# Performance work log

Measured on AMD Instinct MI355X. Metric: run time of the kernel, lower is better.

## Reference

```python
import jax, jax.numpy as jnp
import numpy as np
import math

D_MODEL = 1024
N_HEADS = 16
D_HEAD = D_MODEL // N_HEADS
B, T = 2, 2048


def setup_inputs() -> dict:
    key = jax.random.key(0)
    ks = jax.random.split(key, 5)
    x = jax.random.normal(ks[0], (B, T, D_MODEL), dtype=jnp.float32)
    W_qkv = jax.random.normal(ks[1], (D_MODEL, 3 * D_MODEL), dtype=jnp.float32) * 0.02
    b_qkv = jnp.zeros((3 * D_MODEL,), dtype=jnp.float32)
    W_g = jax.random.normal(ks[2], (N_HEADS, D_HEAD, D_HEAD), dtype=jnp.float32) * 0.02
    W_out = jax.random.normal(ks[3], (D_MODEL, D_MODEL), dtype=jnp.float32) * 0.02
    b_out = jnp.zeros((D_MODEL,), dtype=jnp.float32)
    return {"x": x, "W_qkv": W_qkv, "b_qkv": b_qkv, "W_g": W_g, "W_out": W_out, "b_out": b_out}


def reference(x, W_qkv, b_qkv, W_g, W_out, b_out):
    b, t, d = x.shape
    h, dh = N_HEADS, D_HEAD
    qkv = x @ W_qkv + b_qkv                         # (B,T,3D)
    q, k, v = jnp.split(qkv, 3, axis=-1)
    # (B,T,D) -> (B,H,T,dh)
    q = q.reshape(b, t, h, dh).transpose(0, 2, 1, 3)
    k = k.reshape(b, t, h, dh).transpose(0, 2, 1, 3)
    v = v.reshape(b, t, h, dh).transpose(0, 2, 1, 3)
    scale = 1.0 / math.sqrt(dh)
    scores = jnp.einsum('bhtd,bhsd->bhts', q, k) * scale   # (B,H,T,T)
    causal = jnp.tril(jnp.ones((t, t), dtype=bool))
    scores = jnp.where(causal, scores, jnp.float32(-jnp.inf))
    attn = jax.nn.softmax(scores, axis=-1)
    # query-conditioned bilinear value gate (applied at each position)
    g = jax.nn.sigmoid(jnp.einsum('bhtd,hde->bhte', q, W_g))  # (B,H,T,dh)
    v = g * v
    out = jnp.einsum('bhts,bhsd->bhtd', attn, v)             # (B,H,T,dh)
    out = out.transpose(0, 2, 1, 3).reshape(b, t, d)
    return out @ W_out + b_out
```

## Files before the change

kernel.cpp:

```cpp
#include <hip/hip_runtime.h>
#include <hip/hip_bf16.h>

typedef unsigned short ushortT;
typedef __bf16 bf16x8 __attribute__((ext_vector_type(8)));
typedef __bf16 bf16x4 __attribute__((ext_vector_type(4)));
typedef float f32x4 __attribute__((ext_vector_type(4)));

#define T_SEQ 2048
#define DH 64
#define NH 16
#define DM 1024
#define TD 3072
#define BATCH 2
#define LOG2E 1.44269504f

__device__ inline ushortT f2bf(float f){
    union { float f; unsigned int u; } a; a.f = f;
    unsigned int r = a.u + 0x7fffu + ((a.u >> 16) & 1u);
    return (ushortT)(r >> 16);
}
__device__ inline float bf2f(ushortT u){
    union { float f; unsigned int u; } a; a.u = ((unsigned int)u) << 16;
    return a.f;
}

__device__ inline void gload_lds16(const void* g, void* l){
    __builtin_amdgcn_global_load_lds((const __attribute__((address_space(1))) void*)g,
                                     (__attribute__((address_space(3))) void*)l, 16, 0, 0);
}

__global__ __launch_bounds__(256) void cast_bf16_kernel(const float* __restrict__ in,
                                                        ushortT* __restrict__ out, int n){
    int i = (blockIdx.x * 256 + threadIdx.x) * 4;
    if (i < n){
        float4 v = *(const float4*)&in[i];
        out[i+0] = f2bf(v.x); out[i+1] = f2bf(v.y);
        out[i+2] = f2bf(v.z); out[i+3] = f2bf(v.w);
    }
}

__global__ __launch_bounds__(256) void transcast_kernel(const float* __restrict__ in,
                                                        ushortT* __restrict__ out, int K, int N){
    __shared__ float tile[64][65];
    int n0 = blockIdx.x * 64, k0 = blockIdx.y * 64;
    int tid = threadIdx.x;
    int c  = tid & 63;
    int r4 = tid >> 6;
#pragma unroll
    for (int i = 0; i < 16; i++){
        int k = r4 + i * 4;
        tile[k][c] = in[(size_t)(k0 + k) * N + n0 + c];
    }
    __syncthreads();
#pragma unroll
    for (int i = 0; i < 16; i++){
        int n = r4 + i * 4;
        out[(size_t)(n0 + n) * K + k0 + c] = f2bf(tile[c][n]);
    }
}

__global__ __launch_bounds__(256) void wg_transcast_kernel(const float* __restrict__ in,
                                                           ushortT* __restrict__ out){
    __shared__ float tile[64][65];
    int h = blockIdx.x;
    int tid = threadIdx.x;
    int c = tid & 63, r4 = tid >> 6;
#pragma unroll
    for (int i = 0; i < 16; i++){
        int d = r4 + i*4;
        tile[d][c] = in[h*4096 + d*64 + c];
    }
    __syncthreads();
#pragma unroll
    for (int i = 0; i < 16; i++){
        int e = r4 + i*4;
        out[h*4096 + e*64 + c] = f2bf(tile[c][e]);
    }
}

__device__ inline void store_out(ushortT* C, size_t i, float v){ C[i] = f2bf(v); }
__device__ inline void store_out(float*   C, size_t i, float v){ C[i] = v; }

template <typename OUT>
__global__ __launch_bounds__(256) void gemm_bf16_kernel(const ushortT* __restrict__ A,
                                                        const ushortT* __restrict__ BT,
                                                        const float* __restrict__ bias,
                                                        OUT* __restrict__ C,
                                                        int M, int N, int K){
    __shared__ __align__(16) ushortT As[2][128*32];
    __shared__ __align__(16) ushortT Bs[2][128*32];
    int tid = threadIdx.x;
    int m0 = blockIdx.x * 128;
    int n0 = blockIdx.y * 128;
    int wid = tid >> 6, lane = tid & 63;
    int l15 = lane & 15, g = lane >> 4;
    int wr = wid >> 1, wc = wid & 1;

    f32x4 acc[4][4];
#pragma unroll
    for (int i = 0; i < 4; i++)
#pragma unroll
        for (int j = 0; j < 4; j++) acc[i][j] = (f32x4){0.f,0.f,0.f,0.f};

    int srow = wid * 32 + (lane >> 2);
    int sch  = lane & 3;

#define GSTAGE(buf, k0)                                                                  \
    {                                                                                    \
        _Pragma("unroll")                                                                \
        for (int i_ = 0; i_ < 2; i_++){                                                  \
            int row_ = srow + i_ * 16;                                                   \
            const ushortT* asrc_ = A  + (size_t)(m0 + row_) * K + (k0) + sch * 8;        \
            const ushortT* bsrc_ = BT + (size_t)(n0 + row_) * K + (k0) + sch * 8;        \
            gload_lds16(asrc_, (char*)As[buf] + (wid*2 + i_) * 1024);                    \
            gload_lds16(bsrc_, (char*)Bs[buf] + (wid*2 + i_) * 1024);                    \
        }                                                                                \
    }

    GSTAGE(0, 0);
    __syncthreads();

    int nk = K >> 5;
    for (int kt = 0; kt < nk; kt++){
        int buf = kt & 1;
        if (kt + 1 < nk) GSTAGE(buf ^ 1, (kt + 1) * 32);

        bf16x8 af[4], bfr[4];
#pragma unroll
        for (int mi = 0; mi < 4; mi++){
            int r = wr*64 + mi*16 + l15;
            af[mi]  = *(const bf16x8*)(As[buf] + r*32 + g*8);
        }
#pragma unroll
        for (int ni = 0; ni < 4; ni++){
            int r = wc*64 + ni*16 + l15;
            bfr[ni] = *(const bf16x8*)(Bs[buf] + r*32 + g*8);
        }
#pragma unroll
        for (int mi = 0; mi < 4; mi++)
#pragma unroll
            for (int ni = 0; ni < 4; ni++)
                acc[mi][ni] = __builtin_amdgcn_mfma_f32_16x16x32_bf16(af[mi], bfr[ni], acc[mi][ni], 0, 0, 0);
        __syncthreads();
    }
#undef GSTAGE

#pragma unroll
    for (int mi = 0; mi < 4; mi++){
#pragma unroll
        for (int jj = 0; jj < 4; jj++){
            int mm = m0 + wr*64 + mi*16 + 4*g + jj;
#pragma unroll
            for (int ni = 0; ni < 4; ni++){
                int nn = n0 + wc*64 + ni*16 + l15;
                float v = acc[mi][ni][jj] + bias[nn];
                store_out(C, (size_t)mm * N + nn, v);
            }
        }
    }
}

__global__ __launch_bounds__(256) void gate_kernel(const ushortT* __restrict__ qkv,
                                                   const ushortT* __restrict__ WgT,
                                                   ushortT* __restrict__ vgT){
    __shared__ __align__(16) ushortT VT[64][72];
    int tblk = blockIdx.x, bh = blockIdx.y;
    int b = bh >> 4, h = bh & 15;
    int tid = threadIdx.x, wid = tid >> 6, lane = tid & 63;
    int l15 = lane & 15, g = lane >> 4;
    int t0 = tblk * 64;
    int tl = wid*16 + l15;

    const ushortT* qrow = qkv + ((size_t)b*T_SEQ + t0 + tl)*TD + h*DH;
    bf16x8 qf0 = *(const bf16x8*)(qrow + 8*g);
    bf16x8 qf1 = *(const bf16x8*)(qrow + 32 + 8*g);

    const ushortT* wbase = WgT + h*4096;
    const ushortT* vrow = qkv + ((size_t)b*T_SEQ + t0 + tl)*TD + 2*DM + h*DH;

#pragma unroll
    for (int ns = 0; ns < 4; ns++){
        int e = ns*16 + l15;
        bf16x8 wf0 = *(const bf16x8*)(wbase + e*64 + 8*g);
        bf16x8 wf1 = *(const bf16x8*)(wbase + e*64 + 32 + 8*g);
        f32x4 z = (f32x4){0.f,0.f,0.f,0.f};
        z = __builtin_amdgcn_mfma_f32_16x16x32_bf16(wf0, qf0, z, 0, 0, 0);
        z = __builtin_amdgcn_mfma_f32_16x16x32_bf16(wf1, qf1, z, 0, 0, 0);
        union { ushortT u[4]; uint2 v; } v4;
        v4.v = *(const uint2*)(vrow + ns*16 + 4*g);
#pragma unroll
        for (int jj = 0; jj < 4; jj++){
            float ex = __builtin_amdgcn_exp2f(-z[jj] * LOG2E);
            float gv = __builtin_amdgcn_rcpf(1.f + ex);
            VT[ns*16 + 4*g + jj][tl] = f2bf(gv * bf2f(v4.u[jj]));
        }
    }
    __syncthreads();
    for (int i = tid; i < 64*8; i += 256){
        int e = i >> 3, c8 = (i & 7) * 8;
        *(uint4*)&vgT[((size_t)bh * DH + e) * T_SEQ + t0 + c8] = *(const uint4*)&VT[e][c8];
    }
}

struct QState {
    bf16x8 qf0, qf1;
    float m_, lsum;
    f32x4 acc[4];
};

__device__ __forceinline__ void proc_tile(const ushortT* __restrict__ Kb,
                                          const ushortT* __restrict__ Vb,
                                          QState& S, bool diag,
                                          int wid, int l15, int g,
                                          ushortT (*Pl)[72], float* Al){
    f32x4 s[4];
    __builtin_amdgcn_s_setprio(1);
#pragma unroll
    for (int ns = 0; ns < 4; ns++){
        int kr = ns*16 + l15;
        bf16x8 kf0 = *(const bf16x8*)(Kb + kr*64 + ((g     ) ^ (kr & 7))*8);
        bf16x8 kf1 = *(const bf16x8*)(Kb + kr*64 + ((4 + g) ^ (kr & 7))*8);
        f32x4 z = (f32x4){0.f,0.f,0.f,0.f};
        z = __builtin_amdgcn_mfma_f32_16x16x32_bf16(kf0, S.qf0, z, 0, 0, 0);
        z = __builtin_amdgcn_mfma_f32_16x16x32_bf16(kf1, S.qf1, z, 0, 0, 0);
        s[ns] = z;
    }
    __builtin_amdgcn_s_setprio(0);

    float tmax = -INFINITY;
    if (diag){
        int qrel = wid*16 + l15;
#pragma unroll
        for (int ns = 0; ns < 4; ns++){
            int kbase = ns*16 + 4*g;
#pragma unroll
            for (int jj = 0; jj < 4; jj++){
                if (kbase + jj > qrel) s[ns][jj] = -INFINITY;
                tmax = fmaxf(tmax, s[ns][jj]);
            }
        }
    } else {
#pragma unroll
        for (int ns = 0; ns < 4; ns++){
            float a = fmaxf(s[ns][0], s[ns][1]);
            float c = fmaxf(s[ns][2], s[ns][3]);
            tmax = fmaxf(tmax, fmaxf(a, c));
        }
    }
    tmax = fmaxf(tmax, __shfl_xor(tmax, 16, 64));
    tmax = fmaxf(tmax, __shfl_xor(tmax, 32, 64));

    float mnew = fmaxf(S.m_, tmax);
    float mc = mnew * LOG2E;
    float rs = 0.f;
#pragma unroll
    for (int ns = 0; ns < 4; ns++){
        bf16x4 pk;
#pragma unroll
        for (int jj = 0; jj < 4; jj++){
            float p = __builtin_amdgcn_exp2f(fmaf(s[ns][jj], LOG2E, -mc));
            pk[jj] = (__bf16)p;
            rs += p;
        }
        *(bf16x4*)&Pl[l15][ns*16 + 4*g] = pk;
    }
    rs += __shfl_xor(rs, 16, 64);
    rs += __shfl_xor(rs, 32, 64);

    if (!__all(mnew == S.m_)){
        float alpha = __builtin_amdgcn_exp2f(fmaf(S.m_, LOG2E, -mc));
        Al[l15] = alpha;
        f32x4 a4 = *(const f32x4*)&Al[4*g];
#pragma unroll
        for (int nt = 0; nt < 4; nt++)
#pragma unroll
            for (int jj = 0; jj < 4; jj++) S.acc[nt][jj] *= a4[jj];
        S.lsum *= alpha;
        S.m_ = mnew;
    }
    S.lsum += rs;

    __builtin_amdgcn_s_setprio(1);
#pragma unroll
    for (int ks = 0; ks < 2; ks++){
        bf16x8 pa = *(const bf16x8*)&Pl[l15][ks*32 + 8*g];
#pragma unroll
        for (int nt = 0; nt < 4; nt++){
            int e = nt*16 + l15;
            bf16x8 vf = *(const bf16x8*)(Vb + e*64 + ((ks*4 + g) ^ (e & 7))*8);
            S.acc[nt] = __builtin_amdgcn_mfma_f32_16x16x32_bf16(pa, vf, S.acc[nt], 0, 0, 0);
        }
    }
    __builtin_amdgcn_s_setprio(0);
}

__global__ __launch_bounds__(256) void attn_kernel(const ushortT* __restrict__ qkv,
                                                   const ushortT* __restrict__ vgT,
                                                   ushortT* __restrict__ obf){
    __shared__ __align__(16) ushortT Ks[2][64*64];
    __shared__ __align__(16) ushortT Vs[2][64*64];
    __shared__ __align__(16) ushortT Plds[2][4][16][72];
    __shared__ __align__(16) float Alds[2][4][16];
    int bh = blockIdx.x, pairid = blockIdx.y;
    int b = bh >> 4, h = bh & 15;
    int tid = threadIdx.x, wid = tid >> 6, lane = tid & 63;
    int l15 = lane & 15, g = lane >> 4;

    const ushortT* Kg = qkv + (size_t)b * T_SEQ * TD + DM + h * DH;
    const ushortT* Vg = vgT + (size_t)bh * DH * T_SEQ;

    int st_row = wid*16 + (lane >> 3);
    int st_c   = lane & 7;

#define STAGE_TILE(bufidx, kv0)                                                          \
    {                                                                                    \
        _Pragma("unroll")                                                                \
        for (int i_ = 0; i_ < 2; i_++){                                                  \
            int row_ = st_row + i_*8;                                                    \
            int sc_  = st_c ^ (row_ & 7);                                                \
            const ushortT* ksrc_ = Kg + (size_t)((kv0) + row_) * TD + sc_*8;             \
            const ushortT* vsrc_ = Vg + (size_t)row_ * T_SEQ + (kv0) + sc_*8;            \
            gload_lds16(ksrc_, (char*)Ks[bufidx] + (wid*2 + i_)*1024);                   \
            gload_lds16(vsrc_, (char*)Vs[bufidx] + (wid*2 + i_)*1024);                   \
        }                                                                                \
    }

    int pA = pairid, pB = 31 - pairid;

    QState SA, SB;
    {
        int qrow = pA*64 + wid*16 + l15;
        const ushortT* qb = qkv + ((size_t)b * T_SEQ + qrow) * TD + h * DH;
        SA.qf0 = *(const bf16x8*)(qb + 8*g);
        SA.qf1 = *(const bf16x8*)(qb + 32 + 8*g);
    }
    {
        int qrow = pB*64 + wid*16 + l15;
        const ushortT* qb = qkv + ((size_t)b * T_SEQ + qrow) * TD + h * DH;
        SB.qf0 = *(const bf16x8*)(qb + 8*g);
        SB.qf1 = *(const bf16x8*)(qb + 32 + 8*g);
    }
#pragma unroll
    for (int j = 0; j < 8; j++){
        SA.qf0[j] = (__bf16)((float)SA.qf0[j] * 0.125f);
        SA.qf1[j] = (__bf16)((float)SA.qf1[j] * 0.125f);
        SB.qf0[j] = (__bf16)((float)SB.qf0[j] * 0.125f);
        SB.qf1[j] = (__bf16)((float)SB.qf1[j] * 0.125f);
    }
    SA.m_ = -INFINITY; SA.lsum = 0.f;
    SB.m_ = -INFINITY; SB.lsum = 0.f;
#pragma unroll
    for (int nt = 0; nt < 4; nt++){
        SA.acc[nt] = (f32x4){0.f,0.f,0.f,0.f};
        SB.acc[nt] = (f32x4){0.f,0.f,0.f,0.f};
    }

    STAGE_TILE(0, 0);
    __syncthreads();

    for (int t = 0; t <= pB; t++){
        int buf = t & 1;
        if (t < pB) STAGE_TILE(buf ^ 1, (t+1)*64);
        const ushortT* Kb = Ks[buf];
        const ushortT* Vb = Vs[buf];
        if (t <= pA)
            proc_tile(Kb, Vb, SA, t == pA, wid, l15, g, Plds[0][wid], Alds[0][wid]);
        proc_tile(Kb, Vb, SB, t == pB, wid, l15, g, Plds[1][wid], Alds[1][wid]);
        __syncthreads();
    }
#undef STAGE_TILE

    {
        Alds[0][wid][l15] = 1.f / SA.lsum;
        f32x4 i4 = *(const f32x4*)&Alds[0][wid][4*g];
#pragma unroll
        for (int jj = 0; jj < 4; jj++){
            int t = pA*64 + wid*16 + 4*g + jj;
#pragma unroll
            for (int nt = 0; nt < 4; nt++)
                obf[((size_t)b * T_SEQ + t) * DM + h*DH + nt*16 + l15] =
                    f2bf(SA.acc[nt][jj] * i4[jj]);
        }
    }
    {
        Alds[1][wid][l15] = 1.f / SB.lsum;
        f32x4 i4 = *(const f32x4*)&Alds[1][wid][4*g];
#pragma unroll
        for (int jj = 0; jj < 4; jj++){
            int t = pB*64 + wid*16 + 4*g + jj;
#pragma unroll
            for (int nt = 0; nt < 4; nt++)
                obf[((size_t)b * T_SEQ + t) * DM + h*DH + nt*16 + l15] =
                    f2bf(SB.acc[nt][jj] * i4[jj]);
        }
    }
}

extern "C" void kernel_launch(void* const* d_in, const int* in_sizes, int n_in,
                              void* d_out, int out_size, void* d_ws, size_t ws_size,
                              hipStream_t stream){
    const float* x    = (const float*)d_in[0];
    const float* Wqkv = (const float*)d_in[1];
    const float* bqkv = (const float*)d_in[2];
    const float* Wg   = (const float*)d_in[3];
    const float* Wout = (const float*)d_in[4];
    const float* bout = (const float*)d_in[5];

    char* ws = (char*)d_ws;
    ushortT* xbf   = (ushortT*)(ws);
    ushortT* wqkvT = (ushortT*)(ws + 8388608);
    ushortT* woutT = (ushortT*)(ws + 14680064);
    ushortT* qkvb  = (ushortT*)(ws + 16777216);
    ushortT* vgT   = (ushortT*)(ws + 41943040);
    ushortT* obf   = (ushortT*)(ws + 50331648);
    ushortT* wgT   = (ushortT*)(ws + 58720256);

    cast_bf16_kernel<<<4096, 256, 0, stream>>>(x, xbf, 4194304);
    transcast_kernel<<<dim3(48,16), 256, 0, stream>>>(Wqkv, wqkvT, 1024, 3072);
    transcast_kernel<<<dim3(16,16), 256, 0, stream>>>(Wout, woutT, 1024, 1024);
    wg_transcast_kernel<<<16, 256, 0, stream>>>(Wg, wgT);
    gemm_bf16_kernel<ushortT><<<dim3(32,24), 256, 0, stream>>>(xbf, wqkvT, bqkv, qkvb, 4096, 3072, 1024);
    gate_kernel<<<dim3(32,32), 256, 0, stream>>>(qkvb, wgT, vgT);
    attn_kernel<<<dim3(32,16), 256, 0, stream>>>(qkvb, vgT, obf);
    gemm_bf16_kernel<float><<<dim3(32,8), 256, 0, stream>>>(obf, woutT, bout, (float*)d_out, 4096, 1024, 1024);
}
```

Measured before the change: 131.2 us.

## Split paired query tiles across two wave groups in 512-thread attention blocks

The attention kernel now launches 512 threads per block. Waves 0-3 handle the early query tile and waves 4-7 the late one, instead of each of 4 waves processing both tiles in turn. K/V staging is spread over 8 waves with one 16-byte load each. The goal is more concurrent waves per block and less per-wave serial work and register pressure. The cost is that the early-tile group sits idle at barriers after it finishes its causal range, while the late group keeps working.

```diff
diff --git a/kernel.cpp b/kernel.cpp
--- a/kernel.cpp
+++ b/kernel.cpp
@@ -211,7 +211,7 @@
 __device__ __forceinline__ void proc_tile(const ushortT* __restrict__ Kb,
                                           const ushortT* __restrict__ Vb,
                                           QState& S, bool diag,
-                                          int wid, int l15, int g,
+                                          int wg, int l15, int g,
                                           ushortT (*Pl)[72], float* Al){
     f32x4 s[4];
     __builtin_amdgcn_s_setprio(1);
@@ -229,7 +229,7 @@
 
     float tmax = -INFINITY;
     if (diag){
-        int qrel = wid*16 + l15;
+        int qrel = wg*16 + l15;
 #pragma unroll
         for (int ns = 0; ns < 4; ns++){
             int kbase = ns*16 + 4*g;
@@ -294,66 +294,51 @@
     __builtin_amdgcn_s_setprio(0);
 }
 
-__global__ __launch_bounds__(256) void attn_kernel(const ushortT* __restrict__ qkv,
+__global__ __launch_bounds__(512) void attn_kernel(const ushortT* __restrict__ qkv,
                                                    const ushortT* __restrict__ vgT,
                                                    ushortT* __restrict__ obf){
     __shared__ __align__(16) ushortT Ks[2][64*64];
     __shared__ __align__(16) ushortT Vs[2][64*64];
-    __shared__ __align__(16) ushortT Plds[2][4][16][72];
-    __shared__ __align__(16) float Alds[2][4][16];
+    __shared__ __align__(16) ushortT Plds[8][16][72];
+    __shared__ __align__(16) float Alds[8][16];
     int bh = blockIdx.x, pairid = blockIdx.y;
     int b = bh >> 4, h = bh & 15;
     int tid = threadIdx.x, wid = tid >> 6, lane = tid & 63;
     int l15 = lane & 15, g = lane >> 4;
+    int grp = wid >> 2, wg = wid & 3;
 
     const ushortT* Kg = qkv + (size_t)b * T_SEQ * TD + DM + h * DH;
     const ushortT* Vg = vgT + (size_t)bh * DH * T_SEQ;
 
-    int st_row = wid*16 + (lane >> 3);
-    int st_c   = lane & 7;
+    int st_row = wid*8 + (lane >> 3);
+    int st_c   = (lane & 7) ^ ((lane >> 3) & 7);
 
 #define STAGE_TILE(bufidx, kv0)                                                          \
     {                                                                                    \
-        _Pragma("unroll")                                                                \
-        for (int i_ = 0; i_ < 2; i_++){                                                  \
-            int row_ = st_row + i_*8;                                                    \
-            int sc_  = st_c ^ (row_ & 7);                                                \
-            const ushortT* ksrc_ = Kg + (size_t)((kv0) + row_) * TD + sc_*8;             \
-            const ushortT* vsrc_ = Vg + (size_t)row_ * T_SEQ + (kv0) + sc_*8;            \
-            gload_lds16(ksrc_, (char*)Ks[bufidx] + (wid*2 + i_)*1024);                   \
-            gload_lds16(vsrc_, (char*)Vs[bufidx] + (wid*2 + i_)*1024);                   \
-        }                                                                                \
+        const ushortT* ksrc_ = Kg + (size_t)((kv0) + st_row) * TD + st_c*8;              \
+        const ushortT* vsrc_ = Vg + (size_t)st_row * T_SEQ + (kv0) + st_c*8;             \
+        gload_lds16(ksrc_, (char*)Ks[bufidx] + wid*1024);                                \
+        gload_lds16(vsrc_, (char*)Vs[bufidx] + wid*1024);                                \
     }
 
     int pA = pairid, pB = 31 - pairid;
-
-    QState SA, SB;
+    int myp = grp ? pB : pA;
+
+    QState S;
     {
-        int qrow = pA*64 + wid*16 + l15;
+        int qrow = myp*64 + wg*16 + l15;
         const ushortT* qb = qkv + ((size_t)b * T_SEQ + qrow) * TD + h * DH;
-        SA.qf0 = *(const bf16x8*)(qb + 8*g);
-        SA.qf1 = *(const bf16x8*)(qb + 32 + 8*g);
-    }
-    {
-        int qrow = pB*64 + wid*16 + l15;
-        const ushortT* qb = qkv + ((size_t)b * T_SEQ + qrow) * TD + h * DH;
-        SB.qf0 = *(const bf16x8*)(qb + 8*g);
-        SB.qf1 = *(const bf16x8*)(qb + 32 + 8*g);
+        S.qf0 = *(const bf16x8*)(qb + 8*g);
+        S.qf1 = *(const bf16x8*)(qb + 32 + 8*g);
     }
 #pragma unroll
     for (int j = 0; j < 8; j++){
-        SA.qf0[j] = (__bf16)((float)SA.qf0[j] * 0.125f);
-        SA.qf1[j] = (__bf16)((float)SA.qf1[j] * 0.125f);
-        SB.qf0[j] = (__bf16)((float)SB.qf0[j] * 0.125f);
-        SB.qf1[j] = (__bf16)((float)SB.qf1[j] * 0.125f);
-    }
-    SA.m_ = -INFINITY; SA.lsum = 0.f;
-    SB.m_ = -INFINITY; SB.lsum = 0.f;
-#pragma unroll
-    for (int nt = 0; nt < 4; nt++){
-        SA.acc[nt] = (f32x4){0.f,0.f,0.f,0.f};
-        SB.acc[nt] = (f32x4){0.f,0.f,0.f,0.f};
-    }
+        S.qf0[j] = (__bf16)((float)S.qf0[j] * 0.125f);
+        S.qf1[j] = (__bf16)((float)S.qf1[j] * 0.125f);
+    }
+    S.m_ = -INFINITY; S.lsum = 0.f;
+#pragma unroll
+    for (int nt = 0; nt < 4; nt++) S.acc[nt] = (f32x4){0.f,0.f,0.f,0.f};
 
     STAGE_TILE(0, 0);
     __syncthreads();
@@ -361,38 +346,21 @@
     for (int t = 0; t <= pB; t++){
         int buf = t & 1;
         if (t < pB) STAGE_TILE(buf ^ 1, (t+1)*64);
-        const ushortT* Kb = Ks[buf];
-        const ushortT* Vb = Vs[buf];
-        if (t <= pA)
-            proc_tile(Kb, Vb, SA, t == pA, wid, l15, g, Plds[0][wid], Alds[0][wid]);
-        proc_tile(Kb, Vb, SB, t == pB, wid, l15, g, Plds[1][wid], Alds[1][wid]);
+        if (t <= myp)
+            proc_tile(Ks[buf], Vs[buf], S, t == myp, wg, l15, g, Plds[wid], Alds[wid]);
         __syncthreads();
     }
 #undef STAGE_TILE
 
-    {
-        Alds[0][wid][l15] = 1.f / SA.lsum;
-        f32x4 i4 = *(const f32x4*)&Alds[0][wid][4*g];
-#pragma unroll
-        for (int jj = 0; jj < 4; jj++){
-            int t = pA*64 + wid*16 + 4*g + jj;
-#pragma unroll
-            for (int nt = 0; nt < 4; nt++)
-                obf[((size_t)b * T_SEQ + t) * DM + h*DH + nt*16 + l15] =
-                    f2bf(SA.acc[nt][jj] * i4[jj]);
-        }
-    }
-    {
-        Alds[1][wid][l15] = 1.f / SB.lsum;
-        f32x4 i4 = *(const f32x4*)&Alds[1][wid][4*g];
-#pragma unroll
-        for (int jj = 0; jj < 4; jj++){
-            int t = pB*64 + wid*16 + 4*g + jj;
-#pragma unroll
-            for (int nt = 0; nt < 4; nt++)
-                obf[((size_t)b * T_SEQ + t) * DM + h*DH + nt*16 + l15] =
-                    f2bf(SB.acc[nt][jj] * i4[jj]);
-        }
+    Alds[wid][l15] = 1.f / S.lsum;
+    f32x4 i4 = *(const f32x4*)&Alds[wid][4*g];
+#pragma unroll
+    for (int jj = 0; jj < 4; jj++){
+        int t = myp*64 + wg*16 + 4*g + jj;
+#pragma unroll
+        for (int nt = 0; nt < 4; nt++)
+            obf[((size_t)b * T_SEQ + t) * DM + h*DH + nt*16 + l15] =
+                f2bf(S.acc[nt][jj] * i4[jj]);
     }
 }
 
@@ -421,6 +389,6 @@
     wg_transcast_kernel<<<16, 256, 0, stream>>>(Wg, wgT);
     gemm_bf16_kernel<ushortT><<<dim3(32,24), 256, 0, stream>>>(xbf, wqkvT, bqkv, qkvb, 4096, 3072, 1024);
     gate_kernel<<<dim3(32,32), 256, 0, stream>>>(qkvb, wgT, vgT);
-    attn_kernel<<<dim3(32,16), 256, 0, stream>>>(qkvb, vgT, obf);
+    attn_kernel<<<dim3(32,16), 512, 0, stream>>>(qkvb, vgT, obf);
     gemm_bf16_kernel<float><<<dim3(32,8), 256, 0, stream>>>(obf, woutT, bout, (float*)d_out, 4096, 1024, 1024);
 }
```

Result: faster. 126.4 us (-3.7%).
